# Optimization experiments

Hardware: AMD Instinct MI355X
Metric: run time of the kernel (lower is better)

## Reference

```python
import jax, jax.numpy as jnp
import numpy as np

NUM_HEADS = 12
TOP_K = 4
LN_EPS = 1e-5


def _ln(x, w, b):
    m = jnp.mean(x, -1, keepdims=True)
    v = jnp.mean((x - m) ** 2, -1, keepdims=True)
    return (x - m) * jax.lax.rsqrt(v + LN_EPS) * w + b


def _attn(x, qkv_w, qkv_b, proj_w, proj_b):
    B, N, C = x.shape
    hd = C // NUM_HEADS
    qkv = (x @ qkv_w + qkv_b).reshape(B, N, 3, NUM_HEADS, hd)
    q, k, v = jnp.moveaxis(qkv, 2, 0)  # each [B,N,H,hd]
    attn = jax.nn.softmax(jnp.einsum('bnhd,bmhd->bhnm', q * hd ** -0.5, k), axis=-1)
    out = jnp.einsum('bhnm,bmhd->bnhd', attn, v).reshape(B, N, C)
    return out @ proj_w + proj_b


def _moe(x2, gate_w, w1, b1, w2, b2):
    # x2: [tokens, D]; vmoe-style token top-k gating (eval mode, no noise)
    Tt = x2.shape[0]
    E = gate_w.shape[1]
    probs = jax.nn.softmax(x2 @ gate_w, axis=-1)            # [tokens, E]
    topv, topi = jax.lax.top_k(probs, TOP_K)                # [tokens, K]
    combine = jnp.zeros((Tt, E), x2.dtype).at[jnp.arange(Tt)[:, None], topi].set(topv)
    h = jax.nn.gelu(jnp.einsum('td,edh->teh', x2, w1) + b1[None], approximate=False)
    y = jnp.einsum('teh,ehd->ted', h, w2) + b2[None]
    return jnp.einsum('ted,te->td', y, combine)


def reference(x, ln1a_w, ln1a_b, qkv_wa, qkv_ba, proj_wa, proj_ba, ln2a_w, ln2a_b,
              fc1_w, fc1_b, fc2_w, fc2_b,
              ln1b_w, ln1b_b, qkv_wb, qkv_bb, proj_wb, proj_bb, ln2b_w, ln2b_b,
              gate_w, w1, b1, w2, b2, head_w, head_b,
              shared_masks, agg_mask):
    B, N, D = x.shape
    # dense ViT block
    x = x + _attn(_ln(x, ln1a_w, ln1a_b), qkv_wa, qkv_ba, proj_wa, proj_ba)
    h = _ln(x, ln2a_w, ln2a_b)
    x = x + (jax.nn.gelu(h @ fc1_w + fc1_b, approximate=False) @ fc2_w + fc2_b)
    # MoE ViT block
    x = x + _attn(_ln(x, ln1b_w, ln1b_b), qkv_wb, qkv_bb, proj_wb, proj_bb)
    h = _ln(x, ln2b_w, ln2b_b).reshape(B * N, D)
    x = x + _moe(h, gate_w, w1, b1, w2, b2).reshape(B, N, D)
    # per-task heads + masked multi-task aggregation (Aggregation.forward)
    task_out = jnp.einsum('bnd,tdo->tbno', x, head_w) + head_b[:, None, None, :]
    valid = (shared_masks & agg_mask[None]).astype(x.dtype)[..., None]  # [T,B,N,1]
    summed = (task_out * valid).sum(0)
    count = valid.sum(0)
    return summed / (count + 1e-6)


def setup_inputs() -> dict:
    key = jax.random.key(0)
    ks = jax.random.split(key, 32)
    B, N, D, HID, E, T = 8, 197, 768, 3072, 8, 8
    f = lambda k, shape: (jax.random.normal(k, shape, jnp.float32) * 0.02)
    return {
        'x': jax.random.normal(ks[0], (B, N, D), jnp.float32),
        'ln1a_w': jnp.ones((D,)), 'ln1a_b': jnp.zeros((D,)),
        'qkv_wa': f(ks[1], (D, 3 * D)), 'qkv_ba': jnp.zeros((3 * D,)),
        'proj_wa': f(ks[2], (D, D)), 'proj_ba': jnp.zeros((D,)),
        'ln2a_w': jnp.ones((D,)), 'ln2a_b': jnp.zeros((D,)),
        'fc1_w': f(ks[3], (D, HID)), 'fc1_b': jnp.zeros((HID,)),
        'fc2_w': f(ks[4], (HID, D)), 'fc2_b': jnp.zeros((D,)),
        'ln1b_w': jnp.ones((D,)), 'ln1b_b': jnp.zeros((D,)),
        'qkv_wb': f(ks[5], (D, 3 * D)), 'qkv_bb': jnp.zeros((3 * D,)),
        'proj_wb': f(ks[6], (D, D)), 'proj_bb': jnp.zeros((D,)),
        'ln2b_w': jnp.ones((D,)), 'ln2b_b': jnp.zeros((D,)),
        'gate_w': f(ks[7], (D, E)),
        'w1': f(ks[8], (E, D, HID)), 'b1': jnp.zeros((E, HID)),
        'w2': f(ks[9], (E, HID, D)), 'b2': jnp.zeros((E, D)),
        'head_w': f(ks[10], (T, D, D)), 'head_b': jnp.zeros((T, D)),
        'shared_masks': jax.random.bernoulli(ks[11], 0.5, (T, B, N)),
        'agg_mask': jax.random.bernoulli(ks[12], 0.5, (B, N)),
    }
```

## Files before the change

kernel.cpp:

```cpp
#include <hip/hip_runtime.h>
#include <hip/hip_bf16.h>

#define DEV static __device__ __forceinline__

typedef short bfx8 __attribute__((ext_vector_type(8)));
typedef float fx4  __attribute__((ext_vector_type(4)));

DEV float bf2f(__hip_bfloat16 h) { return __bfloat162float(h); }
DEV __hip_bfloat16 f2bf(float f) { return __float2bfloat16(f); }
DEV float uLO(unsigned u) { return __uint_as_float(u << 16); }
DEV unsigned short f2bfu(float f) { __hip_bfloat16 h = __float2bfloat16(f); return *(unsigned short*)&h; }

DEV float wave_sum(float v) {
#pragma unroll
  for (int o = 32; o; o >>= 1) v += __shfl_xor(v, o, 64);
  return v;
}

#define GLD_LDS16(gp, lp) __builtin_amdgcn_global_load_lds( \
    (__attribute__((address_space(1))) void*)(gp),          \
    (__attribute__((address_space(3))) void*)(lp), 16, 0, 0)

struct TDesc { const float* src; __hip_bfloat16* dst; int R, C, nz, tilesPerZ, tileOff; };
struct TPack { TDesc d[9]; int n; };

__global__ __launch_bounds__(256) void transpose_all_k(TPack p) {
  __shared__ float tile[32][33];
  const int bid = blockIdx.x;
  int di = 0;
#pragma unroll
  for (int i = 1; i < 9; ++i)
    if (i < p.n && bid >= p.d[i].tileOff) di = i;
  const TDesc d = p.d[di];
  int local = bid - d.tileOff;
  int z = local / d.tilesPerZ;
  int rem = local - z * d.tilesPerZ;
  int ctiles = d.C >> 5;
  int bx = rem % ctiles, by = rem / ctiles;
  const float* src = d.src + (size_t)z * d.R * d.C;
  __hip_bfloat16* dst = d.dst + (size_t)z * d.R * d.C;
  int c0 = bx * 32, r0 = by * 32;
#pragma unroll
  for (int i = 0; i < 32; i += 8)
    tile[threadIdx.y + i][threadIdx.x] =
        src[(size_t)(r0 + threadIdx.y + i) * d.C + c0 + threadIdx.x];
  __syncthreads();
#pragma unroll
  for (int i = 0; i < 32; i += 8)
    dst[(size_t)(c0 + threadIdx.y + i) * d.R + r0 + threadIdx.x] =
        f2bf(tile[threadIdx.x][threadIdx.y + i]);
}

__global__ __launch_bounds__(256) void transpose_k(
    const float* __restrict__ src, __hip_bfloat16* __restrict__ dst,
    int R, int C)
{
  __shared__ float tile[32][33];
  size_t off = (size_t)blockIdx.z * R * C;
  src += off; dst += off;
  int c0 = blockIdx.x * 32, r0 = blockIdx.y * 32;
#pragma unroll
  for (int i = 0; i < 32; i += 8)
    tile[threadIdx.y + i][threadIdx.x] =
        src[(size_t)(r0 + threadIdx.y + i) * C + c0 + threadIdx.x];
  __syncthreads();
#pragma unroll
  for (int i = 0; i < 32; i += 8)
    dst[(size_t)(c0 + threadIdx.y + i) * R + r0 + threadIdx.x] =
        f2bf(tile[threadIdx.x][threadIdx.y + i]);
}

enum { EPI_STORE = 0, EPI_GELU = 1, EPI_RESADD = 2, EPI_MOE = 3,
       EPI_GELU_R = 4, EPI_MOEP = 5, EPI_HEAD_R = 6 };

template <int MODE>
__global__ __launch_bounds__(256) void gemm_bt(
    const __hip_bfloat16* __restrict__ A,
    const __hip_bfloat16* __restrict__ BT,
    const float* __restrict__ bias,
    int M, int N, int K, int splitK, int taskBase,
    long long strideBz, long long strideBiasz, long long strideAz, long long strideCz,
    __hip_bfloat16* __restrict__ Cb, float* __restrict__ Cf,
    const float* __restrict__ combine, const int* __restrict__ rt)
{
  constexpr bool ROUTED = (MODE == EPI_GELU_R || MODE == EPI_MOEP || MODE == EPI_HEAD_R);
  constexpr bool GATHER = (MODE == EPI_GELU_R || MODE == EPI_HEAD_R);
  __shared__ __hip_bfloat16 sA[2][128 * 32];
  __shared__ __hip_bfloat16 sB[2][128 * 32];
  const int tid = threadIdx.x;
  const int wave = tid >> 6, lane = tid & 63;
  const int quad = lane >> 4, l16 = lane & 15;
  const int z = blockIdx.z;
  const int zt = z / splitK;
  const int kc = z - zt * splitK;
  const int task = taskBase + zt;
  const int Ksub = K / splitK;
  const int kbeg = kc * Ksub;
  const int m0 = blockIdx.y * 128, n0 = blockIdx.x * 128;

  int Meff = M;
  int rtb = 0;
  const int* ilist = nullptr;
  if (ROUTED) {
    const int base = (MODE == EPI_HEAD_R) ? 8 : 0;
    Meff = rt[base + zt];
    ilist = rt + 24 + (size_t)base * M + (size_t)zt * M;
    if (MODE == EPI_MOEP) rtb = rt[16 + zt];
    if (m0 >= Meff) return;
  }

  A += (size_t)zt * strideAz;
  if (MODE != EPI_MOEP) Cb += (size_t)zt * strideCz;
  const __hip_bfloat16* Bz = BT + (size_t)zt * strideBz;
  const float* biasz = bias + (size_t)zt * strideBiasz;
  const int wm = (wave >> 1) * 64, wn = (wave & 1) * 64;

  fx4 acc[4][4];
#pragma unroll
  for (int i = 0; i < 4; ++i)
#pragma unroll
    for (int j = 0; j < 4; ++j) acc[i][j] = (fx4){0.f, 0.f, 0.f, 0.f};

  const int c0 = tid, c1 = tid + 256;
  const int mlim = Meff - 1;
  int gm0 = m0 + (c0 >> 2); if (gm0 > mlim) gm0 = mlim;
  int gm1 = m0 + (c1 >> 2); if (gm1 > mlim) gm1 = mlim;
  const int ar0 = GATHER ? ilist[gm0] : gm0;
  const int ar1 = GATHER ? ilist[gm1] : gm1;
  const int ak0 = (c0 & 3) * 8, ak1 = (c1 & 3) * 8;
  const __hip_bfloat16* pa0 = A + (size_t)ar0 * K + kbeg + ak0;
  const __hip_bfloat16* pa1 = A + (size_t)ar1 * K + kbeg + ak1;
  const __hip_bfloat16* pb0 = Bz + (size_t)(n0 + (c0 >> 2)) * K + kbeg + ak0;
  const __hip_bfloat16* pb1 = Bz + (size_t)(n0 + (c1 >> 2)) * K + kbeg + ak1;

  GLD_LDS16(pa0, &sA[0][c0 * 8]);
  GLD_LDS16(pa1, &sA[0][c1 * 8]);
  GLD_LDS16(pb0, &sB[0][c0 * 8]);
  GLD_LDS16(pb1, &sB[0][c1 * 8]);
  __syncthreads();

  int cur = 0;
  for (int kk = 0; kk < Ksub; kk += 32) {
    const int nxt = kk + 32;
    if (nxt < Ksub) {
      GLD_LDS16(pa0 + nxt, &sA[cur ^ 1][c0 * 8]);
      GLD_LDS16(pa1 + nxt, &sA[cur ^ 1][c1 * 8]);
      GLD_LDS16(pb0 + nxt, &sB[cur ^ 1][c0 * 8]);
      GLD_LDS16(pb1 + nxt, &sB[cur ^ 1][c1 * 8]);
    }
    bfx8 af[4], bfr[4];
#pragma unroll
    for (int i = 0; i < 4; ++i)
      af[i] = *(const bfx8*)(&sA[cur][(wm + i * 16 + l16) * 32 + quad * 8]);
#pragma unroll
    for (int j = 0; j < 4; ++j)
      bfr[j] = *(const bfx8*)(&sB[cur][(wn + j * 16 + l16) * 32 + quad * 8]);
#pragma unroll
    for (int i = 0; i < 4; ++i)
#pragma unroll
      for (int j = 0; j < 4; ++j)
        acc[i][j] = __builtin_amdgcn_mfma_f32_16x16x32_bf16(af[i], bfr[j], acc[i][j], 0, 0, 0);
    __syncthreads();
    cur ^= 1;
  }

  const int mb = m0 + wm + quad * 4;
  const int nb = n0 + wn + l16;
#pragma unroll
  for (int i = 0; i < 4; ++i) {
#pragma unroll
    for (int rr = 0; rr < 4; ++rr) {
      const int m = mb + i * 16 + rr;
      if (m >= Meff) continue;
      int orow = m;
      if (MODE == EPI_HEAD_R) orow = ilist[m];
#pragma unroll
      for (int j = 0; j < 4; ++j) {
        const int n = nb + j * 16;
        float v = acc[i][j][rr];
        if (MODE == EPI_STORE) {
          Cb[(size_t)m * N + n] = f2bf(v + biasz[n]);
        } else if (MODE == EPI_GELU || MODE == EPI_GELU_R) {
          float t = v + biasz[n];
          Cb[(size_t)m * N + n] = f2bf(0.5f * t * (1.f + erff(t * 0.70710678118654752f)));
        } else if (MODE == EPI_RESADD) {
          if (kc == 0) v += biasz[n];
          atomicAdd(&Cf[(size_t)m * N + n], v);
        } else if (MODE == EPI_MOE) {
          float s = combine[m * 8 + task];
          if (s != 0.f) {
            if (kc == 0) v += biasz[n];
            atomicAdd(&Cf[(size_t)m * N + n], s * v);
          }
        } else if (MODE == EPI_MOEP) {
          if (kc == 0) v += biasz[n];
          Cf[(size_t)kc * strideCz + (size_t)(rtb + m) * N + n] = v;
        } else {
          atomicAdd(&Cf[(size_t)orow * N + n], v + biasz[n]);
        }
      }
    }
  }
}

__global__ __launch_bounds__(256) void attn_mfma_k(
    const __hip_bfloat16* __restrict__ qkvb, __hip_bfloat16* __restrict__ outb)
{
  __shared__ __align__(16) unsigned short VT[64 * 232];
  __shared__ __align__(16) unsigned short Pst[4][16 * 232];
  const int tid = threadIdx.x;
  const int chunk = blockIdx.x & 3;
  const int bh = blockIdx.x >> 2;
  const int b = bh / 12, h = bh - b * 12;
  const size_t tokBase = (size_t)b * 197;
  const __hip_bfloat16* qkvh = qkvb + tokBase * 2304 + (size_t)h * 64;

  for (int idx = tid; idx < 197 * 32; idx += 256) {
    int j = idx >> 5, dp = idx & 31;
    unsigned pv = *(const unsigned*)(qkvh + (size_t)j * 2304 + 1536 + dp * 2);
    VT[(2 * dp) * 232 + j]     = (unsigned short)(pv & 0xffffu);
    VT[(2 * dp + 1) * 232 + j] = (unsigned short)(pv >> 16);
  }
  for (int idx = tid; idx < 64 * 35; idx += 256) {
    int r = idx / 35, c = 197 + idx % 35;
    VT[r * 232 + c] = 0;
  }
  __syncthreads();

  const int wave = tid >> 6, lane = tid & 63;
  const int quad = lane >> 4, l16 = lane & 15;
  const int mt = chunk * 4 + wave;
  if (mt >= 13) return;

  {
    int r = lane >> 2, c = 208 + (lane & 3) * 4;
    *(uint2*)&Pst[wave][r * 232 + c] = (uint2){0u, 0u};
  }

  int tq = mt * 16 + l16; if (tq > 196) tq = 196;
  const bfx8 af0 = *(const bfx8*)(qkvh + (size_t)tq * 2304 + quad * 8);
  const bfx8 af1 = *(const bfx8*)(qkvh + (size_t)tq * 2304 + 32 + quad * 8);

  fx4 sv[13];
#pragma unroll
  for (int n0 = 0; n0 < 13; ++n0) {
    int tk = n0 * 16 + l16; if (tk > 196) tk = 196;
    const __hip_bfloat16* kp = qkvh + (size_t)tk * 2304 + 768;
    bfx8 bf0 = *(const bfx8*)(kp + quad * 8);
    bfx8 bf1 = *(const bfx8*)(kp + 32 + quad * 8);
    fx4 a = (fx4){0.f, 0.f, 0.f, 0.f};
    a = __builtin_amdgcn_mfma_f32_16x16x32_bf16(af0, bf0, a, 0, 0, 0);
    a = __builtin_amdgcn_mfma_f32_16x16x32_bf16(af1, bf1, a, 0, 0, 0);
    sv[n0] = a;
  }

  float inv[4];
#pragma unroll
  for (int rr = 0; rr < 4; ++rr) {
    float mx = -3.0e38f;
#pragma unroll
    for (int n0 = 0; n0 < 13; ++n0) {
      bool ok = (n0 < 12) | (l16 < 5);
      float s = ok ? sv[n0][rr] * 0.125f : -3.0e38f;
      sv[n0][rr] = s;
      mx = fmaxf(mx, s);
    }
#pragma unroll
    for (int o = 1; o < 16; o <<= 1) mx = fmaxf(mx, __shfl_xor(mx, o, 64));
    float sum = 0.f;
#pragma unroll
    for (int n0 = 0; n0 < 13; ++n0) {
      float s = sv[n0][rr];
      float e = (s > -1.0e38f) ? __expf(s - mx) : 0.f;
      sv[n0][rr] = e;
      sum += e;
    }
#pragma unroll
    for (int o = 1; o < 16; o <<= 1) sum += __shfl_xor(sum, o, 64);
    inv[rr] = 1.f / sum;
    const int row = quad * 4 + rr;
#pragma unroll
    for (int n0 = 0; n0 < 13; ++n0)
      Pst[wave][row * 232 + n0 * 16 + l16] = f2bfu(sv[n0][rr]);
  }

  fx4 pv[4];
#pragma unroll
  for (int nd = 0; nd < 4; ++nd) pv[nd] = (fx4){0.f, 0.f, 0.f, 0.f};
#pragma unroll
  for (int kk = 0; kk < 7; ++kk) {
    bfx8 paf = *(const bfx8*)&Pst[wave][l16 * 232 + kk * 32 + quad * 8];
#pragma unroll
    for (int nd = 0; nd < 4; ++nd) {
      bfx8 bfv = *(const bfx8*)&VT[(nd * 16 + l16) * 232 + kk * 32 + quad * 8];
      pv[nd] = __builtin_amdgcn_mfma_f32_16x16x32_bf16(paf, bfv, pv[nd], 0, 0, 0);
    }
  }

#pragma unroll
  for (int rr = 0; rr < 4; ++rr) {
    const int row = quad * 4 + rr;
#pragma unroll
    for (int n0 = 0; n0 < 13; ++n0) {
      float e = sv[n0][rr];
      Pst[wave][row * 232 + n0 * 16 + l16] = f2bfu(e - uLO(f2bfu(e)));
    }
  }

#pragma unroll
  for (int kk = 0; kk < 7; ++kk) {
    bfx8 paf = *(const bfx8*)&Pst[wave][l16 * 232 + kk * 32 + quad * 8];
#pragma unroll
    for (int nd = 0; nd < 4; ++nd) {
      bfx8 bfv = *(const bfx8*)&VT[(nd * 16 + l16) * 232 + kk * 32 + quad * 8];
      pv[nd] = __builtin_amdgcn_mfma_f32_16x16x32_bf16(paf, bfv, pv[nd], 0, 0, 0);
    }
  }

#pragma unroll
  for (int rr = 0; rr < 4; ++rr) {
    int m = mt * 16 + quad * 4 + rr;
    if (m > 196) continue;
    __hip_bfloat16* op = outb + (tokBase + m) * 768 + (size_t)h * 64;
#pragma unroll
    for (int nd = 0; nd < 4; ++nd)
      op[nd * 16 + l16] = f2bf(pv[nd][rr] * inv[rr]);
  }
}

__global__ __launch_bounds__(256) void ln_k(
    const float* __restrict__ xf, const float* __restrict__ w,
    const float* __restrict__ b, __hip_bfloat16* __restrict__ out, int T)
{
  int wv = threadIdx.x >> 6, lane = threadIdx.x & 63;
  int t = blockIdx.x * 4 + wv;
  if (t >= T) return;
  const float* row = xf + (size_t)t * 768;
  float v[12]; float s = 0.f;
#pragma unroll
  for (int i = 0; i < 12; ++i) { v[i] = row[lane + i * 64]; s += v[i]; }
  s = wave_sum(s);
  float mean = s * (1.f / 768.f);
  float q = 0.f;
#pragma unroll
  for (int i = 0; i < 12; ++i) { float d = v[i] - mean; q += d * d; }
  q = wave_sum(q);
  float rstd = rsqrtf(q * (1.f / 768.f) + 1e-5f);
#pragma unroll
  for (int i = 0; i < 12; ++i) {
    int d = lane + i * 64;
    out[(size_t)t * 768 + d] = f2bf((v[i] - mean) * rstd * w[d] + b[d]);
  }
}

__global__ __launch_bounds__(256) void gate_k(
    const float* __restrict__ xf, const float* __restrict__ lw,
    const float* __restrict__ lb, const float* __restrict__ gw,
    float* __restrict__ combine, int* __restrict__ rt, int* __restrict__ smap,
    __hip_bfloat16* __restrict__ lnbout, int T)
{
  int wv = threadIdx.x >> 6, lane = threadIdx.x & 63;
  int t = blockIdx.x * 4 + wv;
  if (t >= T) return;
  const float* row = xf + (size_t)t * 768;
  float v[12]; float s = 0.f;
#pragma unroll
  for (int i = 0; i < 12; ++i) { v[i] = row[lane + i * 64]; s += v[i]; }
  s = wave_sum(s);
  float mean = s * (1.f / 768.f);
  float qv = 0.f;
#pragma unroll
  for (int i = 0; i < 12; ++i) { float d = v[i] - mean; qv += d * d; }
  qv = wave_sum(qv);
  float rstd = rsqrtf(qv * (1.f / 768.f) + 1e-5f);
  float acc[8];
#pragma unroll
  for (int e = 0; e < 8; ++e) acc[e] = 0.f;
#pragma unroll
  for (int i = 0; i < 12; ++i) {
    int d = lane + i * 64;
    float xn = (v[i] - mean) * rstd * lw[d] + lb[d];
    lnbout[(size_t)t * 768 + d] = f2bf(xn);
    float4 g0 = *(const float4*)(gw + (size_t)d * 8);
    float4 g1 = *(const float4*)(gw + (size_t)d * 8 + 4);
    acc[0] += xn * g0.x; acc[1] += xn * g0.y;
    acc[2] += xn * g0.z; acc[3] += xn * g0.w;
    acc[4] += xn * g1.x; acc[5] += xn * g1.y;
    acc[6] += xn * g1.z; acc[7] += xn * g1.w;
  }
#pragma unroll
  for (int e = 0; e < 8; ++e) acc[e] = wave_sum(acc[e]);
  float mx = acc[0];
#pragma unroll
  for (int e = 1; e < 8; ++e) mx = fmaxf(mx, acc[e]);
  float p[8]; float se = 0.f;
#pragma unroll
  for (int e = 0; e < 8; ++e) { p[e] = __expf(acc[e] - mx); se += p[e]; }
  float inv = 1.f / se;
#pragma unroll
  for (int e = 0; e < 8; ++e) p[e] *= inv;
  float outv[8]; bool used[8];
#pragma unroll
  for (int e = 0; e < 8; ++e) { outv[e] = 0.f; used[e] = false; }
  for (int k = 0; k < 4; ++k) {
    int best = -1; float bv = -1.f;
#pragma unroll
    for (int e = 0; e < 8; ++e) if (!used[e] && p[e] > bv) { bv = p[e]; best = e; }
#pragma unroll
    for (int e = 0; e < 8; ++e) if (e == best) { used[e] = true; outv[e] = bv; }
  }
#pragma unroll
  for (int e = 0; e < 8; ++e) if (lane == e) combine[(size_t)t * 8 + e] = outv[e];
#pragma unroll
  for (int e = 0; e < 8; ++e)
    if (lane == e && outv[e] != 0.f) {
      int slot = atomicAdd(&rt[e], 1);
      rt[24 + e * T + slot] = t;
      smap[(size_t)t * 8 + e] = slot;
    }
}

__global__ void prefix_k(int* __restrict__ rt) {
  if (threadIdx.x == 0) {
    int s = 0;
#pragma unroll
    for (int e = 0; e < 8; ++e) { rt[16 + e] = s; s += rt[e]; }
  }
}

__global__ __launch_bounds__(256) void combine_k(
    const float* __restrict__ y, const float* __restrict__ combine,
    const int* __restrict__ rt, const int* __restrict__ smap,
    float* __restrict__ xf, __hip_bfloat16* __restrict__ lnbout, int T, int CAP)
{
  int wv = threadIdx.x >> 6, lane = threadIdx.x & 63;
  int t = blockIdx.x * 4 + wv;
  if (t >= T) return;
  float acc[12];
#pragma unroll
  for (int i = 0; i < 12; ++i) acc[i] = 0.f;
  for (int e = 0; e < 8; ++e) {
    float s = combine[(size_t)t * 8 + e];
    if (s != 0.f) {
      int r = rt[16 + e] + smap[(size_t)t * 8 + e];
      const float* y0 = y + (size_t)r * 768;
      const float* y1 = y0 + (size_t)CAP * 768;
#pragma unroll
      for (int i = 0; i < 12; ++i)
        acc[i] += s * (y0[lane + i * 64] + y1[lane + i * 64]);
    }
  }
  float* xr = xf + (size_t)t * 768;
#pragma unroll
  for (int i = 0; i < 12; ++i) {
    float nv = xr[lane + i * 64] + acc[i];
    xr[lane + i * 64] = nv;
    lnbout[(size_t)t * 768 + lane + i * 64] = f2bf(nv);
  }
}

__global__ void mask_k(const int* __restrict__ sm, const int* __restrict__ am,
                       float* __restrict__ cnt, int* __restrict__ rt, int T)
{
  int t = blockIdx.x * 256 + threadIdx.x;
  if (t >= T) return;
  int a = am[t] != 0;
  float c = 0.f;
#pragma unroll
  for (int tt = 0; tt < 8; ++tt) {
    int vv = (sm[tt * T + t] != 0) & a;
    if (vv) {
      int slot = atomicAdd(&rt[8 + tt], 1);
      rt[24 + 8 * T + tt * T + slot] = t;
    }
    c += (float)vv;
  }
  cnt[t] = c;
}

__global__ void f2b_k(const float* __restrict__ in, __hip_bfloat16* __restrict__ out, int n) {
  int i = blockIdx.x * 256 + threadIdx.x;
  if (i < n) out[i] = f2bf(in[i]);
}
__global__ void final_k(float* __restrict__ out, const float* __restrict__ cnt, int n) {
  int i = blockIdx.x * 256 + threadIdx.x;
  if (i < n) out[i] = out[i] / (cnt[i / 768] + 1e-6f);
}

extern "C" void kernel_launch(void* const* d_in, const int* in_sizes, int n_in,
                              void* d_out, int out_size, void* d_ws, size_t ws_size,
                              hipStream_t stream)
{
  (void)in_sizes; (void)n_in; (void)out_size;
  const int Ttok = 8 * 197;
  const int D = 768, HID = 3072;
  const int CAP = 4 * Ttok;

  const float* x       = (const float*)d_in[0];
  const float* ln1a_w  = (const float*)d_in[1];
  const float* ln1a_b  = (const float*)d_in[2];
  const float* qkv_wa  = (const float*)d_in[3];
  const float* qkv_ba  = (const float*)d_in[4];
  const float* proj_wa = (const float*)d_in[5];
  const float* proj_ba = (const float*)d_in[6];
  const float* ln2a_w  = (const float*)d_in[7];
  const float* ln2a_b  = (const float*)d_in[8];
  const float* fc1_w   = (const float*)d_in[9];
  const float* fc1_b   = (const float*)d_in[10];
  const float* fc2_w   = (const float*)d_in[11];
  const float* fc2_b   = (const float*)d_in[12];
  const float* ln1b_w  = (const float*)d_in[13];
  const float* ln1b_b  = (const float*)d_in[14];
  const float* qkv_wb  = (const float*)d_in[15];
  const float* qkv_bb  = (const float*)d_in[16];
  const float* proj_wb = (const float*)d_in[17];
  const float* proj_bb = (const float*)d_in[18];
  const float* ln2b_w  = (const float*)d_in[19];
  const float* ln2b_b  = (const float*)d_in[20];
  const float* gate_w  = (const float*)d_in[21];
  const float* w1      = (const float*)d_in[22];
  const float* b1      = (const float*)d_in[23];
  const float* w2      = (const float*)d_in[24];
  const float* b2      = (const float*)d_in[25];
  const float* head_w  = (const float*)d_in[26];
  const float* head_b  = (const float*)d_in[27];
  const int* shared_masks = (const int*)d_in[28];
  const int* agg_mask     = (const int*)d_in[29];
  float* out           = (float*)d_out;

  char* wsp = (char*)d_ws;
  auto alloc = [&](size_t bytes) { char* p = wsp; wsp += (bytes + 255) & ~(size_t)255; return p; };
  float* xf             = (float*)alloc((size_t)Ttok * D * 4);
  __hip_bfloat16* lnb   = (__hip_bfloat16*)alloc((size_t)Ttok * D * 2);
  __hip_bfloat16* qkvb  = (__hip_bfloat16*)alloc((size_t)Ttok * 3 * D * 2);
  __hip_bfloat16* attnb = (__hip_bfloat16*)alloc((size_t)Ttok * D * 2);
  __hip_bfloat16* h1    = (__hip_bfloat16*)alloc((size_t)Ttok * HID * 2);
  float* combine        = (float*)alloc((size_t)Ttok * 8 * 4);
  float* cnt            = (float*)alloc((size_t)Ttok * 4);
  int* rt               = (int*)alloc((size_t)(24 + 16 * Ttok) * 4);
  int* smap             = (int*)alloc((size_t)Ttok * 8 * 4);
  __hip_bfloat16* qkvaT = (__hip_bfloat16*)alloc((size_t)D * 3 * D * 2);
  __hip_bfloat16* projaT= (__hip_bfloat16*)alloc((size_t)D * D * 2);
  __hip_bfloat16* fc1T  = (__hip_bfloat16*)alloc((size_t)D * HID * 2);
  __hip_bfloat16* fc2T  = (__hip_bfloat16*)alloc((size_t)D * HID * 2);
  __hip_bfloat16* qkvbT = (__hip_bfloat16*)alloc((size_t)D * 3 * D * 2);
  __hip_bfloat16* projbT= (__hip_bfloat16*)alloc((size_t)D * D * 2);
  __hip_bfloat16* headT = (__hip_bfloat16*)alloc((size_t)8 * D * D * 2);
  __hip_bfloat16* wT    = (__hip_bfloat16*)alloc((size_t)D * HID * 2);

  const size_t used = (size_t)(wsp - (char*)d_ws);
  const size_t extraNeed = 2 * ((size_t)8 * D * HID * 2 + 255)
                         + ((size_t)8 * Ttok * HID * 2 + 255)
                         + (2 * (size_t)CAP * D * 4 + 255);
  const bool batched = (ws_size >= used + extraNeed);
  __hip_bfloat16* w1T8 = nullptr; __hip_bfloat16* w2T8 = nullptr; __hip_bfloat16* h1_8 = nullptr;
  float* yb = nullptr;
  if (batched) {
    w1T8 = (__hip_bfloat16*)alloc((size_t)8 * D * HID * 2);
    w2T8 = (__hip_bfloat16*)alloc((size_t)8 * D * HID * 2);
    h1_8 = (__hip_bfloat16*)alloc((size_t)8 * Ttok * HID * 2);
    yb   = (float*)alloc(2 * (size_t)CAP * D * 4);
  }

  dim3 tb(32, 8);
  if (batched) {
    TPack p; int off = 0;
    auto addT = [&](int i, const float* s, __hip_bfloat16* dd, int R, int C, int nz) {
      int tpz = (R / 32) * (C / 32);
      p.d[i] = TDesc{s, dd, R, C, nz, tpz, off};
      off += tpz * nz;
    };
    addT(0, qkv_wa, qkvaT, D, 3 * D, 1);
    addT(1, proj_wa, projaT, D, D, 1);
    addT(2, fc1_w, fc1T, D, HID, 1);
    addT(3, fc2_w, fc2T, HID, D, 1);
    addT(4, qkv_wb, qkvbT, D, 3 * D, 1);
    addT(5, proj_wb, projbT, D, D, 1);
    addT(6, head_w, headT, D, D, 8);
    addT(7, w1, w1T8, D, HID, 8);
    addT(8, w2, w2T8, HID, D, 8);
    p.n = 9;
    transpose_all_k<<<off, tb, 0, stream>>>(p);
  } else {
    transpose_k<<<dim3(3*D/32, D/32, 1), tb, 0, stream>>>(qkv_wa, qkvaT, D, 3*D);
    transpose_k<<<dim3(D/32, D/32, 1),   tb, 0, stream>>>(proj_wa, projaT, D, D);
    transpose_k<<<dim3(HID/32, D/32, 1), tb, 0, stream>>>(fc1_w, fc1T, D, HID);
    transpose_k<<<dim3(D/32, HID/32, 1), tb, 0, stream>>>(fc2_w, fc2T, HID, D);
    transpose_k<<<dim3(3*D/32, D/32, 1), tb, 0, stream>>>(qkv_wb, qkvbT, D, 3*D);
    transpose_k<<<dim3(D/32, D/32, 1),   tb, 0, stream>>>(proj_wb, projbT, D, D);
    transpose_k<<<dim3(D/32, D/32, 8),   tb, 0, stream>>>(head_w, headT, D, D);
  }

  const int nTok = Ttok * D;
  hipMemcpyAsync(xf, x, (size_t)nTok * 4, hipMemcpyDeviceToDevice, stream);
  hipMemsetAsync(rt, 0, 64, stream);
  mask_k<<<(Ttok + 255)/256, 256, 0, stream>>>(shared_masks, agg_mask, cnt, rt, Ttok);
  hipMemsetAsync(out, 0, (size_t)nTok * 4, stream);

  const int lnGrid = (Ttok + 3) / 4;
  dim3 g_qkv(3*D/128, 13, 1);
  dim3 g_proj(D/128, 13, 4);
  dim3 g_fc1(HID/128, 13, 1);
  dim3 g_fc2(D/128, 13, 4);
  dim3 g_head(D/128, 13, 8);
  const int attnGrid = 96 * 4;

  ln_k<<<lnGrid, 256, 0, stream>>>(xf, ln1a_w, ln1a_b, lnb, Ttok);
  gemm_bt<EPI_STORE><<<g_qkv, 256, 0, stream>>>(lnb, qkvaT, qkv_ba, Ttok, 3*D, D, 1, 0, 0, 0, 0, 0, qkvb, nullptr, nullptr, nullptr);
  attn_mfma_k<<<attnGrid, 256, 0, stream>>>(qkvb, attnb);
  gemm_bt<EPI_RESADD><<<g_proj, 256, 0, stream>>>(attnb, projaT, proj_ba, Ttok, D, D, 4, 0, 0, 0, 0, 0, nullptr, xf, nullptr, nullptr);
  ln_k<<<lnGrid, 256, 0, stream>>>(xf, ln2a_w, ln2a_b, lnb, Ttok);
  gemm_bt<EPI_GELU><<<g_fc1, 256, 0, stream>>>(lnb, fc1T, fc1_b, Ttok, HID, D, 1, 0, 0, 0, 0, 0, h1, nullptr, nullptr, nullptr);
  gemm_bt<EPI_RESADD><<<g_fc2, 256, 0, stream>>>(h1, fc2T, fc2_b, Ttok, D, HID, 4, 0, 0, 0, 0, 0, nullptr, xf, nullptr, nullptr);

  ln_k<<<lnGrid, 256, 0, stream>>>(xf, ln1b_w, ln1b_b, lnb, Ttok);
  gemm_bt<EPI_STORE><<<g_qkv, 256, 0, stream>>>(lnb, qkvbT, qkv_bb, Ttok, 3*D, D, 1, 0, 0, 0, 0, 0, qkvb, nullptr, nullptr, nullptr);
  attn_mfma_k<<<attnGrid, 256, 0, stream>>>(qkvb, attnb);
  gemm_bt<EPI_RESADD><<<g_proj, 256, 0, stream>>>(attnb, projbT, proj_bb, Ttok, D, D, 4, 0, 0, 0, 0, 0, nullptr, xf, nullptr, nullptr);
  gate_k<<<lnGrid, 256, 0, stream>>>(xf, ln2b_w, ln2b_b, gate_w, combine, rt, smap, lnb, Ttok);
  prefix_k<<<1, 64, 0, stream>>>(rt);
  if (batched) {
    gemm_bt<EPI_GELU_R><<<dim3(HID/128, 13, 8), 256, 0, stream>>>(
        lnb, w1T8, b1, Ttok, HID, D, 1, 0,
        (long long)D*HID, HID, 0, (long long)Ttok*HID, h1_8, nullptr, nullptr, rt);
    gemm_bt<EPI_MOEP><<<dim3(D/128, 13, 16), 256, 0, stream>>>(
        h1_8, w2T8, b2, Ttok, D, HID, 2, 0,
        (long long)HID*D, D, (long long)Ttok*HID, (long long)CAP*D, nullptr, yb, nullptr, rt);
    combine_k<<<lnGrid, 256, 0, stream>>>(yb, combine, rt, smap, xf, lnb, Ttok, CAP);
  } else {
    for (int e = 0; e < 8; ++e) {
      transpose_k<<<dim3(HID/32, D/32, 1), tb, 0, stream>>>(w1 + (size_t)e*D*HID, wT, D, HID);
      gemm_bt<EPI_GELU><<<g_fc1, 256, 0, stream>>>(lnb, wT, b1 + (size_t)e*HID, Ttok, HID, D, 1, 0, 0, 0, 0, 0, h1, nullptr, nullptr, nullptr);
      transpose_k<<<dim3(D/32, HID/32, 1), tb, 0, stream>>>(w2 + (size_t)e*HID*D, wT, HID, D);
      gemm_bt<EPI_MOE><<<g_fc2, 256, 0, stream>>>(h1, wT, b2 + (size_t)e*D, Ttok, D, HID, 4, e, 0, 0, 0, 0, nullptr, xf, combine, nullptr);
    }
    f2b_k<<<(nTok + 255)/256, 256, 0, stream>>>(xf, lnb, nTok);
  }

  gemm_bt<EPI_HEAD_R><<<g_head, 256, 0, stream>>>(lnb, headT, head_b, Ttok, D, D, 1, 0, (long long)D*D, D, 0, 0, nullptr, out, nullptr, rt);
  final_k<<<(nTok + 255)/256, 256, 0, stream>>>(out, cnt, nTok);
}
```

Measured before the change: 834.3 us.

## Vectorize weight transpose with 64x64 tiles and replace head atomics with packed gather-sum

The batched weight transpose now uses 64x64 tiles. It reads float4 vectors, converts to bf16 before storing to shared memory, and writes 16-byte bf16 vectors. The per-task head GEMM no longer atomically adds into the output. It writes rows densely into a packed buffer indexed by per-task prefix offsets, and a new final kernel gathers and sums each token's valid task rows and divides by the count. This removes the output memset, the float atomics and the separate divide pass. In exchange it adds a slot map, an extra prefix computation and reuse of the yb buffer, which must be large enough for all valid task rows.

```diff
diff --git a/kernel.cpp b/kernel.cpp
--- a/kernel.cpp
+++ b/kernel.cpp
@@ -25,7 +25,7 @@
 struct TPack { TDesc d[9]; int n; };
 
 __global__ __launch_bounds__(256) void transpose_all_k(TPack p) {
-  __shared__ float tile[32][33];
+  __shared__ unsigned short t[64 * 66];
   const int bid = blockIdx.x;
   int di = 0;
 #pragma unroll
@@ -35,20 +35,34 @@
   int local = bid - d.tileOff;
   int z = local / d.tilesPerZ;
   int rem = local - z * d.tilesPerZ;
-  int ctiles = d.C >> 5;
+  int ctiles = d.C >> 6;
   int bx = rem % ctiles, by = rem / ctiles;
   const float* src = d.src + (size_t)z * d.R * d.C;
   __hip_bfloat16* dst = d.dst + (size_t)z * d.R * d.C;
-  int c0 = bx * 32, r0 = by * 32;
-#pragma unroll
-  for (int i = 0; i < 32; i += 8)
-    tile[threadIdx.y + i][threadIdx.x] =
-        src[(size_t)(r0 + threadIdx.y + i) * d.C + c0 + threadIdx.x];
+  int c0 = bx * 64, r0 = by * 64;
+  const int tid = threadIdx.x;
+#pragma unroll
+  for (int it = 0; it < 4; ++it) {
+    int idx = tid + it * 256;
+    int row = idx >> 4, q = idx & 15;
+    float4 v = *(const float4*)(src + (size_t)(r0 + row) * d.C + c0 + q * 4);
+    ushort2 lo, hi;
+    lo.x = f2bfu(v.x); lo.y = f2bfu(v.y);
+    hi.x = f2bfu(v.z); hi.y = f2bfu(v.w);
+    *(ushort2*)&t[row * 66 + q * 4]     = lo;
+    *(ushort2*)&t[row * 66 + q * 4 + 2] = hi;
+  }
   __syncthreads();
 #pragma unroll
-  for (int i = 0; i < 32; i += 8)
-    dst[(size_t)(c0 + threadIdx.y + i) * d.R + r0 + threadIdx.x] =
-        f2bf(tile[threadIdx.x][threadIdx.y + i]);
+  for (int it = 0; it < 2; ++it) {
+    int idx = tid + it * 256;
+    int oc = idx >> 3, q = idx & 7;
+    bfx8 w;
+#pragma unroll
+    for (int j = 0; j < 8; ++j)
+      w[j] = (short)t[(q * 8 + j) * 66 + oc];
+    *(bfx8*)(dst + (size_t)(c0 + oc) * d.R + r0 + q * 8) = w;
+  }
 }
 
 __global__ __launch_bounds__(256) void transpose_k(
@@ -71,7 +85,7 @@
 }
 
 enum { EPI_STORE = 0, EPI_GELU = 1, EPI_RESADD = 2, EPI_MOE = 3,
-       EPI_GELU_R = 4, EPI_MOEP = 5, EPI_HEAD_R = 6 };
+       EPI_GELU_R = 4, EPI_MOEP = 5, EPI_HEAD_R = 6, EPI_HEADP = 7 };
 
 template <int MODE>
 __global__ __launch_bounds__(256) void gemm_bt(
@@ -83,8 +97,9 @@
     __hip_bfloat16* __restrict__ Cb, float* __restrict__ Cf,
     const float* __restrict__ combine, const int* __restrict__ rt)
 {
-  constexpr bool ROUTED = (MODE == EPI_GELU_R || MODE == EPI_MOEP || MODE == EPI_HEAD_R);
-  constexpr bool GATHER = (MODE == EPI_GELU_R || MODE == EPI_HEAD_R);
+  constexpr bool ROUTED = (MODE == EPI_GELU_R || MODE == EPI_MOEP ||
+                           MODE == EPI_HEAD_R || MODE == EPI_HEADP);
+  constexpr bool GATHER = (MODE == EPI_GELU_R || MODE == EPI_HEAD_R || MODE == EPI_HEADP);
   __shared__ __hip_bfloat16 sA[2][128 * 32];
   __shared__ __hip_bfloat16 sB[2][128 * 32];
   const int tid = threadIdx.x;
@@ -102,15 +117,16 @@
   int rtb = 0;
   const int* ilist = nullptr;
   if (ROUTED) {
-    const int base = (MODE == EPI_HEAD_R) ? 8 : 0;
+    const int base = (MODE == EPI_HEAD_R || MODE == EPI_HEADP) ? 8 : 0;
     Meff = rt[base + zt];
-    ilist = rt + 24 + (size_t)base * M + (size_t)zt * M;
+    ilist = rt + 32 + (size_t)base * M + (size_t)zt * M;
     if (MODE == EPI_MOEP) rtb = rt[16 + zt];
+    if (MODE == EPI_HEADP) rtb = rt[24 + zt];
     if (m0 >= Meff) return;
   }
 
   A += (size_t)zt * strideAz;
-  if (MODE != EPI_MOEP) Cb += (size_t)zt * strideCz;
+  if (MODE != EPI_MOEP && MODE != EPI_HEADP) Cb += (size_t)zt * strideCz;
   const __hip_bfloat16* Bz = BT + (size_t)zt * strideBz;
   const float* biasz = bias + (size_t)zt * strideBiasz;
   const int wm = (wave >> 1) * 64, wn = (wave & 1) * 64;
@@ -195,6 +211,8 @@
         } else if (MODE == EPI_MOEP) {
           if (kc == 0) v += biasz[n];
           Cf[(size_t)kc * strideCz + (size_t)(rtb + m) * N + n] = v;
+        } else if (MODE == EPI_HEADP) {
+          Cf[(size_t)(rtb + m) * N + n] = v + biasz[n];
         } else {
           atomicAdd(&Cf[(size_t)orow * N + n], v + biasz[n]);
         }
@@ -415,7 +433,7 @@
   for (int e = 0; e < 8; ++e)
     if (lane == e && outv[e] != 0.f) {
       int slot = atomicAdd(&rt[e], 1);
-      rt[24 + e * T + slot] = t;
+      rt[32 + e * T + slot] = t;
       smap[(size_t)t * 8 + e] = slot;
     }
 }
@@ -425,6 +443,9 @@
     int s = 0;
 #pragma unroll
     for (int e = 0; e < 8; ++e) { rt[16 + e] = s; s += rt[e]; }
+    int s2 = 0;
+#pragma unroll
+    for (int tt = 0; tt < 8; ++tt) { rt[24 + tt] = s2; s2 += rt[8 + tt]; }
   }
 }
 
@@ -460,7 +481,8 @@
 }
 
 __global__ void mask_k(const int* __restrict__ sm, const int* __restrict__ am,
-                       float* __restrict__ cnt, int* __restrict__ rt, int T)
+                       float* __restrict__ cnt, int* __restrict__ rt,
+                       int* __restrict__ tsmap, int* __restrict__ valid, int T)
 {
   int t = blockIdx.x * 256 + threadIdx.x;
   if (t >= T) return;
@@ -469,10 +491,13 @@
 #pragma unroll
   for (int tt = 0; tt < 8; ++tt) {
     int vv = (sm[tt * T + t] != 0) & a;
+    valid[tt * T + t] = vv;
+    int slot = -1;
     if (vv) {
-      int slot = atomicAdd(&rt[8 + tt], 1);
-      rt[24 + 8 * T + tt * T + slot] = t;
-    }
+      slot = atomicAdd(&rt[8 + tt], 1);
+      rt[32 + 8 * T + tt * T + slot] = t;
+    }
+    tsmap[(size_t)t * 8 + tt] = slot;
     c += (float)vv;
   }
   cnt[t] = c;
@@ -485,6 +510,30 @@
 __global__ void final_k(float* __restrict__ out, const float* __restrict__ cnt, int n) {
   int i = blockIdx.x * 256 + threadIdx.x;
   if (i < n) out[i] = out[i] / (cnt[i / 768] + 1e-6f);
+}
+__global__ __launch_bounds__(256) void final2_k(
+    const float* __restrict__ y2, const int* __restrict__ rt,
+    const int* __restrict__ tsmap, const float* __restrict__ cnt,
+    float* __restrict__ out, int T)
+{
+  int wv = threadIdx.x >> 6, lane = threadIdx.x & 63;
+  int t = blockIdx.x * 4 + wv;
+  if (t >= T) return;
+  float acc[12];
+#pragma unroll
+  for (int i = 0; i < 12; ++i) acc[i] = 0.f;
+  for (int tt = 0; tt < 8; ++tt) {
+    int s = tsmap[(size_t)t * 8 + tt];
+    if (s >= 0) {
+      const float* yr = y2 + (size_t)(rt[24 + tt] + s) * 768;
+#pragma unroll
+      for (int i = 0; i < 12; ++i) acc[i] += yr[lane + i * 64];
+    }
+  }
+  float inv = 1.f / (cnt[t] + 1e-6f);
+  float* orow = out + (size_t)t * 768;
+#pragma unroll
+  for (int i = 0; i < 12; ++i) orow[lane + i * 64] = acc[i] * inv;
 }
 
 extern "C" void kernel_launch(void* const* d_in, const int* in_sizes, int n_in,
@@ -537,8 +586,10 @@
   __hip_bfloat16* h1    = (__hip_bfloat16*)alloc((size_t)Ttok * HID * 2);
   float* combine        = (float*)alloc((size_t)Ttok * 8 * 4);
   float* cnt            = (float*)alloc((size_t)Ttok * 4);
-  int* rt               = (int*)alloc((size_t)(24 + 16 * Ttok) * 4);
+  int* rt               = (int*)alloc((size_t)(32 + 16 * Ttok) * 4);
   int* smap             = (int*)alloc((size_t)Ttok * 8 * 4);
+  int* tsmap            = (int*)alloc((size_t)Ttok * 8 * 4);
+  int* valid            = (int*)alloc((size_t)8 * Ttok * 4);
   __hip_bfloat16* qkvaT = (__hip_bfloat16*)alloc((size_t)D * 3 * D * 2);
   __hip_bfloat16* projaT= (__hip_bfloat16*)alloc((size_t)D * D * 2);
   __hip_bfloat16* fc1T  = (__hip_bfloat16*)alloc((size_t)D * HID * 2);
@@ -566,7 +617,7 @@
   if (batched) {
     TPack p; int off = 0;
     auto addT = [&](int i, const float* s, __hip_bfloat16* dd, int R, int C, int nz) {
-      int tpz = (R / 32) * (C / 32);
+      int tpz = (R / 64) * (C / 64);
       p.d[i] = TDesc{s, dd, R, C, nz, tpz, off};
       off += tpz * nz;
     };
@@ -580,7 +631,7 @@
     addT(7, w1, w1T8, D, HID, 8);
     addT(8, w2, w2T8, HID, D, 8);
     p.n = 9;
-    transpose_all_k<<<off, tb, 0, stream>>>(p);
+    transpose_all_k<<<off, 256, 0, stream>>>(p);
   } else {
     transpose_k<<<dim3(3*D/32, D/32, 1), tb, 0, stream>>>(qkv_wa, qkvaT, D, 3*D);
     transpose_k<<<dim3(D/32, D/32, 1),   tb, 0, stream>>>(proj_wa, projaT, D, D);
@@ -593,9 +644,9 @@
 
   const int nTok = Ttok * D;
   hipMemcpyAsync(xf, x, (size_t)nTok * 4, hipMemcpyDeviceToDevice, stream);
-  hipMemsetAsync(rt, 0, 64, stream);
-  mask_k<<<(Ttok + 255)/256, 256, 0, stream>>>(shared_masks, agg_mask, cnt, rt, Ttok);
-  hipMemsetAsync(out, 0, (size_t)nTok * 4, stream);
+  hipMemsetAsync(rt, 0, 128, stream);
+  mask_k<<<(Ttok + 255)/256, 256, 0, stream>>>(shared_masks, agg_mask, cnt, rt, tsmap, valid, Ttok);
+  if (!batched) hipMemsetAsync(out, 0, (size_t)nTok * 4, stream);
 
   const int lnGrid = (Ttok + 3) / 4;
   dim3 g_qkv(3*D/128, 13, 1);
@@ -627,6 +678,8 @@
         h1_8, w2T8, b2, Ttok, D, HID, 2, 0,
         (long long)HID*D, D, (long long)Ttok*HID, (long long)CAP*D, nullptr, yb, nullptr, rt);
     combine_k<<<lnGrid, 256, 0, stream>>>(yb, combine, rt, smap, xf, lnb, Ttok, CAP);
+    gemm_bt<EPI_HEADP><<<g_head, 256, 0, stream>>>(lnb, headT, head_b, Ttok, D, D, 1, 0, (long long)D*D, D, 0, 0, nullptr, yb, nullptr, rt);
+    final2_k<<<lnGrid, 256, 0, stream>>>(yb, rt, tsmap, cnt, out, Ttok);
   } else {
     for (int e = 0; e < 8; ++e) {
       transpose_k<<<dim3(HID/32, D/32, 1), tb, 0, stream>>>(w1 + (size_t)e*D*HID, wT, D, HID);
@@ -635,8 +688,7 @@
       gemm_bt<EPI_MOE><<<g_fc2, 256, 0, stream>>>(h1, wT, b2 + (size_t)e*D, Ttok, D, HID, 4, e, 0, 0, 0, 0, nullptr, xf, combine, nullptr);
     }
     f2b_k<<<(nTok + 255)/256, 256, 0, stream>>>(xf, lnb, nTok);
-  }
-
-  gemm_bt<EPI_HEAD_R><<<g_head, 256, 0, stream>>>(lnb, headT, head_b, Ttok, D, D, 1, 0, (long long)D*D, D, 0, 0, nullptr, out, nullptr, rt);
-  final_k<<<(nTok + 255)/256, 256, 0, stream>>>(out, cnt, nTok);
-}
+    gemm_bt<EPI_HEAD_R><<<g_head, 256, 0, stream>>>(lnb, headT, head_b, Ttok, D, D, 1, 0, (long long)D*D, D, 0, 0, nullptr, out, nullptr, rt);
+    final_k<<<(nTok + 255)/256, 256, 0, stream>>>(out, cnt, nTok);
+  }
+}
```

Result: faster. 816.1 us (-2.2%).
